# Performance work log

Measured on AMD Instinct MI355X. Metric: run time of the kernel, lower is better.

## Reference

```python
import jax, jax.numpy as jnp
import numpy as np

HIDDEN_DIM = 512
SCALE = HIDDEN_DIM ** (-0.5)


def setup_inputs() -> dict:
    key = jax.random.key(0)
    kx, kw = jax.random.split(key)
    x = jax.random.normal(kx, (4, 4096, HIDDEN_DIM), dtype=jnp.float32)
    # nn.Linear weight is [out, in]; y = x @ W.T. We store W in torch layout.
    Wq = jax.random.normal(kw, (HIDDEN_DIM, HIDDEN_DIM), dtype=jnp.float32) * (HIDDEN_DIM ** -0.5)
    return {"x": x, "Wq": Wq}


def reference(x, Wq):
    # Faithful to source: q, k, v all use the SAME q_matrix projection.
    q = jnp.einsum("bcd,ed->bce", x, Wq)  # [B, C, D]
    k = q
    v = q
    scores = jnp.einsum("bcd,bed->bce", q, k) * SCALE  # [B, C, C]
    attn = jax.nn.softmax(scores, axis=-1)
    # dropout p=0.0 -> identity
    y = jnp.einsum("bce,bed->bcd", attn, v)  # [B, C, D]
    return y
```

## Files before the change

### kernel.cpp

```cpp
#include <hip/hip_runtime.h>
#include <stdint.h>

typedef unsigned int u32;
typedef unsigned short u16;
typedef __attribute__((ext_vector_type(8))) short bf16x8;
typedef __attribute__((ext_vector_type(4))) float f32x4;

#define B_ 4
#define S_ 4096
#define D_ 512
#define SCALE_ 0.04419417382415922f

__device__ __forceinline__ u16 f2b(float f) {
  u32 u = __builtin_bit_cast(u32, f);
  return (u16)((u + 0x7FFFu + ((u >> 16) & 1u)) >> 16);
}
__device__ __forceinline__ u16 f2b_fast(float f) {
  u32 u = __builtin_bit_cast(u32, f);
  return (u16)((u + 0x8000u) >> 16);
}
__device__ __forceinline__ void gld16(const void* g, void* l) {
  __builtin_amdgcn_global_load_lds(
      (const __attribute__((address_space(1))) u32*)g,
      (__attribute__((address_space(3))) u32*)l, 16, 0, 0);
}

__global__ __launch_bounds__(256, 1) void qprep(
    const float* __restrict__ W, u16* __restrict__ Wb) {
  int i = (blockIdx.x * 256 + threadIdx.x) * 4;
  float4 a = *(const float4*)(W + i);
  ushort4 o;
  o.x = f2b(a.x); o.y = f2b(a.y); o.z = f2b(a.z); o.w = f2b(a.w);
  *(ushort4*)(Wb + i) = o;
}

__global__ __launch_bounds__(256, 1) void qproj(
    const float* __restrict__ X, const u16* __restrict__ Wb,
    u16* __restrict__ Qr, u16* __restrict__ Qt) {
  __shared__ __align__(16) u16 Wt[2][512 * 64];
  const int tid = threadIdx.x;
  const int wave = tid >> 6, lane = tid & 63;
  const int m16 = lane & 15, quad = lane >> 4;
  const int r0 = blockIdx.x * 64;

  const float* xrow = X + (size_t)(r0 + wave * 16 + m16) * D_;
  bf16x8 af[16];
#pragma unroll
  for (int ks = 0; ks < 16; ++ks) {
    const float* ap = xrow + ks * 32 + quad * 8;
    float4 a0 = ((const float4*)ap)[0];
    float4 a1 = ((const float4*)ap)[1];
    bf16x8 v;
    v[0] = (short)f2b(a0.x); v[1] = (short)f2b(a0.y);
    v[2] = (short)f2b(a0.z); v[3] = (short)f2b(a0.w);
    v[4] = (short)f2b(a1.x); v[5] = (short)f2b(a1.y);
    v[6] = (short)f2b(a1.z); v[7] = (short)f2b(a1.w);
    af[ks] = v;
  }

  f32x4 acc[32];
#pragma unroll
  for (int i = 0; i < 32; ++i) acc[i] = f32x4{};

  auto stage = [&](int kc, int buf) {
#pragma unroll
    for (int t = 0; t < 16; ++t) {
      int e0 = (wave * 16 + t) * 8;
      int e = e0 + (lane >> 3);
      int gb = ((lane & 7) - e) & 7;
      gld16(Wb + (size_t)e * D_ + kc * 64 + gb * 8, &Wt[buf][e0 * 64]);
    }
  };

  stage(0, 0);
  __syncthreads();

  for (int kc = 0; kc < 8; ++kc) {
    if (kc < 7) stage(kc + 1, (kc + 1) & 1);
    const u16* wb = &Wt[kc & 1][0];
#pragma unroll
    for (int kk = 0; kk < 2; ++kk) {
      int jb = quad + 4 * kk;
      bf16x8 a = af[kc * 2 + kk];
#pragma unroll
      for (int nt = 0; nt < 32; ++nt) {
        int e = m16 + nt * 16;
        bf16x8 bf = *(const bf16x8*)(wb + e * 64 + ((jb + e) & 7) * 8);
        acc[nt] = __builtin_amdgcn_mfma_f32_16x16x32_bf16(a, bf, acc[nt], 0, 0, 0);
      }
    }
    __syncthreads();
  }

  const int b = r0 >> 12;
  const int s0 = (r0 & (S_ - 1)) + wave * 16 + quad * 4;
  const int grow = r0 + wave * 16 + quad * 4;
#pragma unroll
  for (int nt = 0; nt < 32; ++nt) {
    int e = nt * 16 + m16;
    u16 h0 = f2b(acc[nt][0]), h1 = f2b(acc[nt][1]);
    u16 h2 = f2b(acc[nt][2]), h3 = f2b(acc[nt][3]);
    Qr[(size_t)(grow + 0) * D_ + e] = h0;
    Qr[(size_t)(grow + 1) * D_ + e] = h1;
    Qr[(size_t)(grow + 2) * D_ + e] = h2;
    Qr[(size_t)(grow + 3) * D_ + e] = h3;
    uint2 pv;
    pv.x = (u32)h0 | ((u32)h1 << 16);
    pv.y = (u32)h2 | ((u32)h3 << 16);
    *(uint2*)(&Qt[((size_t)(b * D_ + e)) * S_ + s0]) = pv;
  }
}

__global__ __launch_bounds__(256, 1) void flashattn(
    const u16* __restrict__ Qrow, const u16* __restrict__ Qt,
    float* __restrict__ Out) {
  __shared__ __align__(16) u16 Kt[64 * 512];
  __shared__ __align__(16) u16 Vt[512 * 64];
  __shared__ __align__(16) u16 Pl[4][16 * 88];

  const int tid = threadIdx.x;
  const int wave = tid >> 6, lane = tid & 63;
  const int m16 = lane & 15, quad = lane >> 4;
  const int qt = blockIdx.x, bb = blockIdx.y;
  const u16* Qb  = Qrow + (size_t)bb * S_ * D_;
  const u16* Qtb = Qt   + (size_t)bb * D_ * S_;

  auto stageK = [&](int kt) {
    const u16* src = Qb + (size_t)(kt * 64) * D_;
#pragma unroll
    for (int t = 0; t < 16; ++t) {
      int n = wave * 16 + t;
      int gb = (lane & ~7) | ((lane + n) & 7);
      gld16(src + (size_t)n * D_ + gb * 8, &Kt[n * 512]);
    }
  };
  auto stageV = [&](int kt) {
    const u16* vsrc = Qtb + kt * 64;
#pragma unroll
    for (int t = 0; t < 16; ++t) {
      int d0 = (wave * 16 + t) * 8;
      int d  = d0 + (lane >> 3);
      int gb = ((lane & 7) + d) & 7;
      gld16(vsrc + (size_t)d * S_ + gb * 8, &Vt[d0 * 64]);
    }
  };

  bf16x8 qf[16];
  {
    const u16* qp = Qb + (size_t)(qt * 64 + wave * 16 + m16) * D_ + quad * 8;
#pragma unroll
    for (int ks = 0; ks < 16; ++ks) qf[ks] = *(const bf16x8*)(qp + ks * 32);
  }

  bf16x8 onesf;
#pragma unroll
  for (int j = 0; j < 8; ++j) onesf[j] = (short)0x3F80;

  f32x4 o[32];
#pragma unroll
  for (int i = 0; i < 32; ++i) o[i] = f32x4{};
  f32x4 ol = f32x4{};
  float mrow[4] = {-1e30f, -1e30f, -1e30f, -1e30f};
  u16* pw = &Pl[wave][0];

  stageK(0);
  __syncthreads();

  for (int kt = 0; kt < 64; ++kt) {
    stageV(kt);

    f32x4 sv[4];
#pragma unroll
    for (int nt = 0; nt < 4; ++nt) {
      f32x4 a = f32x4{};
      int n = m16 + nt * 16;
      const u16* kr = &Kt[n * 512];
#pragma unroll
      for (int ks = 0; ks < 16; ++ks) {
        int jb = quad + 4 * ks;
        int ib = (jb & ~7) | ((jb - n) & 7);
        bf16x8 bf = *(const bf16x8*)(kr + ib * 8);
        a = __builtin_amdgcn_mfma_f32_16x16x32_bf16(qf[ks], bf, a, 0, 0, 0);
      }
      sv[nt] = a;
    }

    float mnew[4], alpha[4];
    int grew = 0;
#pragma unroll
    for (int r = 0; r < 4; ++r) {
      float t = fmaxf(fmaxf(sv[0][r], sv[1][r]), fmaxf(sv[2][r], sv[3][r]));
      t = fmaxf(t, __shfl_xor(t, 1));
      t = fmaxf(t, __shfl_xor(t, 2));
      t = fmaxf(t, __shfl_xor(t, 4));
      t = fmaxf(t, __shfl_xor(t, 8));
      float mn = fmaxf(mrow[r], t);
      mnew[r] = mn;
      grew |= (mn > mrow[r]);
      alpha[r] = __expf((mrow[r] - mn) * SCALE_);
      mrow[r] = mn;
    }
#pragma unroll
    for (int nt = 0; nt < 4; ++nt) {
#pragma unroll
      for (int r = 0; r < 4; ++r) {
        float p = __expf((sv[nt][r] - mnew[r]) * SCALE_);
        pw[(quad * 4 + r) * 88 + nt * 16 + m16] = f2b_fast(p);
      }
    }

    __syncthreads();

    if (kt < 63) stageK(kt + 1);

    if (__ballot(grew) != 0ull) {
#pragma unroll
      for (int dt = 0; dt < 32; ++dt) {
        o[dt][0] *= alpha[0]; o[dt][1] *= alpha[1];
        o[dt][2] *= alpha[2]; o[dt][3] *= alpha[3];
      }
      ol[0] *= alpha[0]; ol[1] *= alpha[1];
      ol[2] *= alpha[2]; ol[3] *= alpha[3];
    }

#pragma unroll
    for (int ks2 = 0; ks2 < 2; ++ks2) {
      bf16x8 pf = *(const bf16x8*)(pw + m16 * 88 + ks2 * 32 + quad * 8);
      int ib = ((quad + 4 * ks2) - m16) & 7;
#pragma unroll
      for (int dt = 0; dt < 32; ++dt) {
        int d = m16 + dt * 16;
        bf16x8 vf = *(const bf16x8*)(&Vt[d * 64 + ib * 8]);
        o[dt] = __builtin_amdgcn_mfma_f32_16x16x32_bf16(pf, vf, o[dt], 0, 0, 0);
      }
      ol = __builtin_amdgcn_mfma_f32_16x16x32_bf16(pf, onesf, ol, 0, 0, 0);
    }

    __syncthreads();
  }

  float inv[4];
#pragma unroll
  for (int r = 0; r < 4; ++r) inv[r] = 1.f / ol[r];
  const int row0 = qt * 64 + wave * 16 + quad * 4;
#pragma unroll
  for (int dt = 0; dt < 32; ++dt) {
    int col = dt * 16 + m16;
    size_t base = ((size_t)bb * S_ + row0) * D_ + col;
    Out[base]           = o[dt][0] * inv[0];
    Out[base + D_]      = o[dt][1] * inv[1];
    Out[base + 2 * D_]  = o[dt][2] * inv[2];
    Out[base + 3 * D_]  = o[dt][3] * inv[3];
  }
}

extern "C" void kernel_launch(void* const* d_in, const int* in_sizes, int n_in,
                              void* d_out, int out_size, void* d_ws, size_t ws_size,
                              hipStream_t stream) {
  (void)in_sizes; (void)n_in; (void)out_size; (void)ws_size;
  const float* X = (const float*)d_in[0];
  const float* W = (const float*)d_in[1];
  float* Out = (float*)d_out;
  u16* Qr = (u16*)d_ws;
  u16* Qt = Qr + (size_t)B_ * S_ * D_;
  u16* Wb = Qt + (size_t)B_ * D_ * S_;

  qprep<<<dim3(256), dim3(256), 0, stream>>>(W, Wb);
  qproj<<<dim3(256), dim3(256), 0, stream>>>(X, Wb, Qr, Qt);
  flashattn<<<dim3(64, 4), dim3(256), 0, stream>>>(Qr, Qt, Out);
}
```

Baseline: 356.0 us.

## Repartition attention waves by key half and D slice, retile projection GEMM

The attention kernel now splits the score computation so each wave pair covers 32 queries times 32 keys with 32x32x16 MFMAs. Row max and sum are combined through LDS, and each wave owns a 128-wide D slice of the output for all 64 queries. This removes the redundant ones-MFMA row sum and cuts per-wave V fragment loads, since P fragments are reused across four M tiles. The cost is extra barriers and LDS traffic for the softmax statistics. The projection kernel is retiled to 128x128 output blocks over a 2D grid with X loads prefetched in registers and a smaller W buffer, which allows two blocks per CU.

```diff
diff --git a/kernel.cpp b/kernel.cpp
--- a/kernel.cpp
+++ b/kernel.cpp
@@ -5,6 +5,7 @@
 typedef unsigned short u16;
 typedef __attribute__((ext_vector_type(8))) short bf16x8;
 typedef __attribute__((ext_vector_type(4))) float f32x4;
+typedef __attribute__((ext_vector_type(16))) float f32x16;
 
 #define B_ 4
 #define S_ 4096
@@ -18,6 +19,10 @@
 __device__ __forceinline__ u16 f2b_fast(float f) {
   u32 u = __builtin_bit_cast(u32, f);
   return (u16)((u + 0x8000u) >> 16);
+}
+__device__ __forceinline__ float b2f(u16 h) {
+  u32 u = ((u32)h) << 16;
+  return __builtin_bit_cast(float, u);
 }
 __device__ __forceinline__ void gld16(const void* g, void* l) {
   __builtin_amdgcn_global_load_lds(
@@ -34,80 +39,97 @@
   *(ushort4*)(Wb + i) = o;
 }
 
-__global__ __launch_bounds__(256, 1) void qproj(
+__global__ __launch_bounds__(256, 2) void qproj(
     const float* __restrict__ X, const u16* __restrict__ Wb,
     u16* __restrict__ Qr, u16* __restrict__ Qt) {
-  __shared__ __align__(16) u16 Wt[2][512 * 64];
+  __shared__ __align__(16) u16 Wt[2][128 * 64];
   const int tid = threadIdx.x;
   const int wave = tid >> 6, lane = tid & 63;
   const int m16 = lane & 15, quad = lane >> 4;
-  const int r0 = blockIdx.x * 64;
-
-  const float* xrow = X + (size_t)(r0 + wave * 16 + m16) * D_;
-  bf16x8 af[16];
-#pragma unroll
-  for (int ks = 0; ks < 16; ++ks) {
-    const float* ap = xrow + ks * 32 + quad * 8;
-    float4 a0 = ((const float4*)ap)[0];
-    float4 a1 = ((const float4*)ap)[1];
-    bf16x8 v;
-    v[0] = (short)f2b(a0.x); v[1] = (short)f2b(a0.y);
-    v[2] = (short)f2b(a0.z); v[3] = (short)f2b(a0.w);
-    v[4] = (short)f2b(a1.x); v[5] = (short)f2b(a1.y);
-    v[6] = (short)f2b(a1.z); v[7] = (short)f2b(a1.w);
-    af[ks] = v;
-  }
-
-  f32x4 acc[32];
-#pragma unroll
-  for (int i = 0; i < 32; ++i) acc[i] = f32x4{};
-
-  auto stage = [&](int kc, int buf) {
-#pragma unroll
-    for (int t = 0; t < 16; ++t) {
-      int e0 = (wave * 16 + t) * 8;
-      int e = e0 + (lane >> 3);
-      int gb = ((lane & 7) - e) & 7;
-      gld16(Wb + (size_t)e * D_ + kc * 64 + gb * 8, &Wt[buf][e0 * 64]);
+  const int r0 = blockIdx.x * 128, n0 = blockIdx.y * 128;
+
+  auto stageW = [&](int kc, int buf) {
+#pragma unroll
+    for (int t = 0; t < 4; ++t) {
+      int p8 = (wave * 4 + t) * 8;
+      int row = p8 + (lane >> 3);
+      int gb = ((lane & 7) + row) & 7;
+      gld16(Wb + (size_t)(n0 + row) * D_ + kc * 64 + gb * 8, &Wt[buf][p8 * 64]);
     }
   };
-
-  stage(0, 0);
+  auto loadX = [&](int kc, float4* xr) {
+#pragma unroll
+    for (int mt = 0; mt < 2; ++mt)
+#pragma unroll
+      for (int kk = 0; kk < 2; ++kk) {
+        const float* p = X + (size_t)(r0 + wave * 32 + mt * 16 + m16) * D_ +
+                         kc * 64 + kk * 32 + quad * 8;
+        xr[(mt * 2 + kk) * 2]     = ((const float4*)p)[0];
+        xr[(mt * 2 + kk) * 2 + 1] = ((const float4*)p)[1];
+      }
+  };
+
+  f32x4 acc[16];
+#pragma unroll
+  for (int i = 0; i < 16; ++i) acc[i] = f32x4{};
+  float4 xr[8], xr2[8];
+
+  loadX(0, xr);
+  stageW(0, 0);
   __syncthreads();
 
   for (int kc = 0; kc < 8; ++kc) {
-    if (kc < 7) stage(kc + 1, (kc + 1) & 1);
-    const u16* wb = &Wt[kc & 1][0];
-#pragma unroll
-    for (int kk = 0; kk < 2; ++kk) {
-      int jb = quad + 4 * kk;
-      bf16x8 a = af[kc * 2 + kk];
-#pragma unroll
-      for (int nt = 0; nt < 32; ++nt) {
-        int e = m16 + nt * 16;
-        bf16x8 bf = *(const bf16x8*)(wb + e * 64 + ((jb + e) & 7) * 8);
-        acc[nt] = __builtin_amdgcn_mfma_f32_16x16x32_bf16(a, bf, acc[nt], 0, 0, 0);
+    if (kc < 7) { stageW(kc + 1, (kc + 1) & 1); loadX(kc + 1, xr2); }
+    bf16x8 afr[4];
+#pragma unroll
+    for (int f = 0; f < 4; ++f) {
+      float4 a0 = xr[f * 2], a1 = xr[f * 2 + 1];
+      bf16x8 v;
+      v[0] = (short)f2b(a0.x); v[1] = (short)f2b(a0.y);
+      v[2] = (short)f2b(a0.z); v[3] = (short)f2b(a0.w);
+      v[4] = (short)f2b(a1.x); v[5] = (short)f2b(a1.y);
+      v[6] = (short)f2b(a1.z); v[7] = (short)f2b(a1.w);
+      afr[f] = v;
+    }
+    const u16* wbase = &Wt[kc & 1][0];
+#pragma unroll
+    for (int nt = 0; nt < 8; ++nt) {
+#pragma unroll
+      for (int kk = 0; kk < 2; ++kk) {
+        int ib = ((kk * 4 + quad) - m16) & 7;
+        bf16x8 bf = *(const bf16x8*)(wbase + (nt * 16 + m16) * 64 + ib * 8);
+#pragma unroll
+        for (int mt = 0; mt < 2; ++mt)
+          acc[mt * 8 + nt] =
+              __builtin_amdgcn_mfma_f32_16x16x32_bf16(afr[mt * 2 + kk], bf, acc[mt * 8 + nt], 0, 0, 0);
       }
     }
+    if (kc < 7) {
+#pragma unroll
+      for (int i = 0; i < 8; ++i) xr[i] = xr2[i];
+    }
     __syncthreads();
   }
 
-  const int b = r0 >> 12;
-  const int s0 = (r0 & (S_ - 1)) + wave * 16 + quad * 4;
-  const int grow = r0 + wave * 16 + quad * 4;
-#pragma unroll
-  for (int nt = 0; nt < 32; ++nt) {
-    int e = nt * 16 + m16;
-    u16 h0 = f2b(acc[nt][0]), h1 = f2b(acc[nt][1]);
-    u16 h2 = f2b(acc[nt][2]), h3 = f2b(acc[nt][3]);
-    Qr[(size_t)(grow + 0) * D_ + e] = h0;
-    Qr[(size_t)(grow + 1) * D_ + e] = h1;
-    Qr[(size_t)(grow + 2) * D_ + e] = h2;
-    Qr[(size_t)(grow + 3) * D_ + e] = h3;
-    uint2 pv;
-    pv.x = (u32)h0 | ((u32)h1 << 16);
-    pv.y = (u32)h2 | ((u32)h3 << 16);
-    *(uint2*)(&Qt[((size_t)(b * D_ + e)) * S_ + s0]) = pv;
+#pragma unroll
+  for (int mt = 0; mt < 2; ++mt) {
+    const int grow = r0 + wave * 32 + mt * 16 + quad * 4;
+    const int b = grow >> 12;
+    const int s0 = grow & (S_ - 1);
+#pragma unroll
+    for (int nt = 0; nt < 8; ++nt) {
+      int e = n0 + nt * 16 + m16;
+      f32x4 a = acc[mt * 8 + nt];
+      u16 h0 = f2b(a[0]), h1 = f2b(a[1]), h2 = f2b(a[2]), h3 = f2b(a[3]);
+      Qr[(size_t)(grow + 0) * D_ + e] = h0;
+      Qr[(size_t)(grow + 1) * D_ + e] = h1;
+      Qr[(size_t)(grow + 2) * D_ + e] = h2;
+      Qr[(size_t)(grow + 3) * D_ + e] = h3;
+      uint2 pv;
+      pv.x = (u32)h0 | ((u32)h1 << 16);
+      pv.y = (u32)h2 | ((u32)h3 << 16);
+      *(uint2*)(&Qt[((size_t)(b * D_ + e)) * S_ + s0]) = pv;
+    }
   }
 }
 
@@ -116,11 +138,17 @@
     float* __restrict__ Out) {
   __shared__ __align__(16) u16 Kt[64 * 512];
   __shared__ __align__(16) u16 Vt[512 * 64];
-  __shared__ __align__(16) u16 Pl[4][16 * 88];
+  __shared__ __align__(16) u16 Psh[64 * 64];
+  __shared__ float mxArr[2][2][32];
+  __shared__ float alphaArr[64];
+  __shared__ float lsumArr[2][2][32];
+  __shared__ int ldsFlag;
 
   const int tid = threadIdx.x;
   const int wave = tid >> 6, lane = tid & 63;
   const int m16 = lane & 15, quad = lane >> 4;
+  const int l5 = lane & 31, half = lane >> 5;
+  const int qg = wave >> 1, kh = wave & 1;
   const int qt = blockIdx.x, bb = blockIdx.y;
   const u16* Qb  = Qrow + (size_t)bb * S_ * D_;
   const u16* Qtb = Qt   + (size_t)bb * D_ * S_;
@@ -145,112 +173,144 @@
     }
   };
 
-  bf16x8 qf[16];
+  bf16x8 qb[32];
   {
-    const u16* qp = Qb + (size_t)(qt * 64 + wave * 16 + m16) * D_ + quad * 8;
-#pragma unroll
-    for (int ks = 0; ks < 16; ++ks) qf[ks] = *(const bf16x8*)(qp + ks * 32);
-  }
-
-  bf16x8 onesf;
-#pragma unroll
-  for (int j = 0; j < 8; ++j) onesf[j] = (short)0x3F80;
+    const u16* qp = Qb + (size_t)(qt * 64 + qg * 32 + l5) * D_ + half * 8;
+#pragma unroll
+    for (int s = 0; s < 32; ++s) qb[s] = *(const bf16x8*)(qp + s * 16);
+  }
 
   f32x4 o[32];
 #pragma unroll
   for (int i = 0; i < 32; ++i) o[i] = f32x4{};
-  f32x4 ol = f32x4{};
-  float mrow[4] = {-1e30f, -1e30f, -1e30f, -1e30f};
-  u16* pw = &Pl[wave][0];
+  float mrow = -1e30f, lrow = 0.f;
 
   stageK(0);
   __syncthreads();
 
   for (int kt = 0; kt < 64; ++kt) {
     stageV(kt);
-
-    f32x4 sv[4];
-#pragma unroll
-    for (int nt = 0; nt < 4; ++nt) {
-      f32x4 a = f32x4{};
-      int n = m16 + nt * 16;
-      const u16* kr = &Kt[n * 512];
-#pragma unroll
-      for (int ks = 0; ks < 16; ++ks) {
-        int jb = quad + 4 * ks;
-        int ib = (jb & ~7) | ((jb - n) & 7);
-        bf16x8 bf = *(const bf16x8*)(kr + ib * 8);
-        a = __builtin_amdgcn_mfma_f32_16x16x32_bf16(qf[ks], bf, a, 0, 0, 0);
+    if (tid == 0) ldsFlag = 0;
+
+    f32x16 c0 = {}, c1 = {};
+    const int n = kh * 32 + l5;
+    const u16* kr = &Kt[(size_t)n * 512];
+#pragma unroll
+    for (int s = 0; s < 32; s += 2) {
+      int g0 = 2 * s + half, g1 = 2 * s + 2 + half;
+      bf16x8 ka0 = *(const bf16x8*)(kr + ((g0 & ~7) | ((g0 - n) & 7)) * 8);
+      bf16x8 ka1 = *(const bf16x8*)(kr + ((g1 & ~7) | ((g1 - n) & 7)) * 8);
+      c0 = __builtin_amdgcn_mfma_f32_32x32x16_bf16(ka0, qb[s], c0, 0, 0, 0);
+      c1 = __builtin_amdgcn_mfma_f32_32x32x16_bf16(ka1, qb[s + 1], c1, 0, 0, 0);
+    }
+    float sc[16];
+#pragma unroll
+    for (int i = 0; i < 16; ++i) sc[i] = c0[i] + c1[i];
+
+    float pmax = sc[0];
+#pragma unroll
+    for (int i = 1; i < 16; ++i) pmax = fmaxf(pmax, sc[i]);
+    pmax = fmaxf(pmax, __shfl_xor(pmax, 32));
+    if (lane < 32) mxArr[qg][kh][lane] = pmax;
+    __syncthreads();
+
+    float mold = mrow;
+    float mn = fmaxf(mold, fmaxf(mxArr[qg][0][l5], mxArr[qg][1][l5]));
+    bool grew = mn > mold;
+    float alpha = __expf((mold - mn) * SCALE_);
+    mrow = mn;
+    if (kh == 0 && lane < 32) alphaArr[qg * 32 + lane] = alpha;
+    if (__ballot(grew) != 0ull && lane == 0) ldsFlag = 1;
+
+    float psum = 0.f;
+    const int q = qg * 32 + l5;
+    u16* prow = &Psh[q * 64];
+#pragma unroll
+    for (int rr = 0; rr < 4; ++rr) {
+      u16 h0 = f2b_fast(__expf((sc[rr * 4 + 0] - mn) * SCALE_));
+      u16 h1 = f2b_fast(__expf((sc[rr * 4 + 1] - mn) * SCALE_));
+      u16 h2 = f2b_fast(__expf((sc[rr * 4 + 2] - mn) * SCALE_));
+      u16 h3 = f2b_fast(__expf((sc[rr * 4 + 3] - mn) * SCALE_));
+      psum += b2f(h0) + b2f(h1) + b2f(h2) + b2f(h3);
+      uint2 pk;
+      pk.x = (u32)h0 | ((u32)h1 << 16);
+      pk.y = (u32)h2 | ((u32)h3 << 16);
+      int phys = (kh * 4 + rr) ^ (q & 7);
+      *(uint2*)(prow + phys * 8 + half * 4) = pk;
+    }
+    psum += __shfl_xor(psum, 32);
+    lrow = lrow * alpha + psum;
+
+    __syncthreads();
+
+    if (kt < 63) stageK(kt + 1);
+
+    int doRescale = ldsFlag;
+    if (doRescale) {
+      float al[16];
+#pragma unroll
+      for (int mt = 0; mt < 4; ++mt)
+#pragma unroll
+        for (int r = 0; r < 4; ++r) al[mt * 4 + r] = alphaArr[mt * 16 + quad * 4 + r];
+#pragma unroll
+      for (int mt = 0; mt < 4; ++mt)
+#pragma unroll
+        for (int nt = 0; nt < 8; ++nt) {
+          o[mt * 8 + nt][0] *= al[mt * 4 + 0];
+          o[mt * 8 + nt][1] *= al[mt * 4 + 1];
+          o[mt * 8 + nt][2] *= al[mt * 4 + 2];
+          o[mt * 8 + nt][3] *= al[mt * 4 + 3];
+        }
+    }
+
+    bf16x8 pf[8];
+#pragma unroll
+    for (int mt = 0; mt < 4; ++mt)
+#pragma unroll
+      for (int ks2 = 0; ks2 < 2; ++ks2) {
+        int qr = mt * 16 + m16;
+        int phys = (ks2 * 4 + quad) ^ (m16 & 7);
+        pf[mt * 2 + ks2] = *(const bf16x8*)(&Psh[qr * 64 + phys * 8]);
       }
-      sv[nt] = a;
-    }
-
-    float mnew[4], alpha[4];
-    int grew = 0;
+#pragma unroll
+    for (int nt = 0; nt < 8; ++nt) {
+      const u16* vrow = &Vt[(size_t)(wave * 128 + nt * 16 + m16) * 64];
+#pragma unroll
+      for (int ks2 = 0; ks2 < 2; ++ks2) {
+        int ib = ((ks2 * 4 + quad) - m16) & 7;
+        bf16x8 vf = *(const bf16x8*)(vrow + ib * 8);
+#pragma unroll
+        for (int mt = 0; mt < 4; ++mt)
+          o[mt * 8 + nt] =
+              __builtin_amdgcn_mfma_f32_16x16x32_bf16(pf[mt * 2 + ks2], vf, o[mt * 8 + nt], 0, 0, 0);
+      }
+    }
+    __syncthreads();
+  }
+
+  if (lane < 32) lsumArr[qg][kh][lane] = lrow;
+  __syncthreads();
+  float linv[16];
+#pragma unroll
+  for (int mt = 0; mt < 4; ++mt)
 #pragma unroll
     for (int r = 0; r < 4; ++r) {
-      float t = fmaxf(fmaxf(sv[0][r], sv[1][r]), fmaxf(sv[2][r], sv[3][r]));
-      t = fmaxf(t, __shfl_xor(t, 1));
-      t = fmaxf(t, __shfl_xor(t, 2));
-      t = fmaxf(t, __shfl_xor(t, 4));
-      t = fmaxf(t, __shfl_xor(t, 8));
-      float mn = fmaxf(mrow[r], t);
-      mnew[r] = mn;
-      grew |= (mn > mrow[r]);
-      alpha[r] = __expf((mrow[r] - mn) * SCALE_);
-      mrow[r] = mn;
-    }
-#pragma unroll
-    for (int nt = 0; nt < 4; ++nt) {
-#pragma unroll
-      for (int r = 0; r < 4; ++r) {
-        float p = __expf((sv[nt][r] - mnew[r]) * SCALE_);
-        pw[(quad * 4 + r) * 88 + nt * 16 + m16] = f2b_fast(p);
-      }
-    }
-
-    __syncthreads();
-
-    if (kt < 63) stageK(kt + 1);
-
-    if (__ballot(grew) != 0ull) {
-#pragma unroll
-      for (int dt = 0; dt < 32; ++dt) {
-        o[dt][0] *= alpha[0]; o[dt][1] *= alpha[1];
-        o[dt][2] *= alpha[2]; o[dt][3] *= alpha[3];
-      }
-      ol[0] *= alpha[0]; ol[1] *= alpha[1];
-      ol[2] *= alpha[2]; ol[3] *= alpha[3];
-    }
-
-#pragma unroll
-    for (int ks2 = 0; ks2 < 2; ++ks2) {
-      bf16x8 pf = *(const bf16x8*)(pw + m16 * 88 + ks2 * 32 + quad * 8);
-      int ib = ((quad + 4 * ks2) - m16) & 7;
-#pragma unroll
-      for (int dt = 0; dt < 32; ++dt) {
-        int d = m16 + dt * 16;
-        bf16x8 vf = *(const bf16x8*)(&Vt[d * 64 + ib * 8]);
-        o[dt] = __builtin_amdgcn_mfma_f32_16x16x32_bf16(pf, vf, o[dt], 0, 0, 0);
-      }
-      ol = __builtin_amdgcn_mfma_f32_16x16x32_bf16(pf, onesf, ol, 0, 0, 0);
-    }
-
-    __syncthreads();
-  }
-
-  float inv[4];
-#pragma unroll
-  for (int r = 0; r < 4; ++r) inv[r] = 1.f / ol[r];
-  const int row0 = qt * 64 + wave * 16 + quad * 4;
-#pragma unroll
-  for (int dt = 0; dt < 32; ++dt) {
-    int col = dt * 16 + m16;
-    size_t base = ((size_t)bb * S_ + row0) * D_ + col;
-    Out[base]           = o[dt][0] * inv[0];
-    Out[base + D_]      = o[dt][1] * inv[1];
-    Out[base + 2 * D_]  = o[dt][2] * inv[2];
-    Out[base + 3 * D_]  = o[dt][3] * inv[3];
+      int qr = mt * 16 + quad * 4 + r;
+      float l = lsumArr[qr >> 5][0][qr & 31] + lsumArr[qr >> 5][1][qr & 31];
+      linv[mt * 4 + r] = 1.f / l;
+    }
+#pragma unroll
+  for (int mt = 0; mt < 4; ++mt) {
+    const int row0 = qt * 64 + mt * 16 + quad * 4;
+#pragma unroll
+    for (int nt = 0; nt < 8; ++nt) {
+      int d = wave * 128 + nt * 16 + m16;
+      size_t base = ((size_t)bb * S_ + row0) * D_ + d;
+      Out[base]          = o[mt * 8 + nt][0] * linv[mt * 4 + 0];
+      Out[base + D_]     = o[mt * 8 + nt][1] * linv[mt * 4 + 1];
+      Out[base + 2 * D_] = o[mt * 8 + nt][2] * linv[mt * 4 + 2];
+      Out[base + 3 * D_] = o[mt * 8 + nt][3] * linv[mt * 4 + 3];
+    }
   }
 }
 
@@ -266,6 +326,6 @@
   u16* Wb = Qt + (size_t)B_ * D_ * S_;
 
   qprep<<<dim3(256), dim3(256), 0, stream>>>(W, Wb);
-  qproj<<<dim3(256), dim3(256), 0, stream>>>(X, Wb, Qr, Qt);
+  qproj<<<dim3(128, 4), dim3(256), 0, stream>>>(X, Wb, Qr, Qt);
   flashattn<<<dim3(64, 4), dim3(256), 0, stream>>>(Qr, Qt, Out);
 }
```

Result: slower. 479.8 us (+34.8%).
